# Optimization experiments

Hardware: AMD Instinct MI355X
Metric: run time of the kernel (lower is better)

## Reference

```python
import jax, jax.numpy as jnp
import numpy as np

B, T, DIM, NH = 2, 2048, 1024, 16
HD = DIM // NH  # 64


def setup_inputs() -> dict:
    key = jax.random.key(0)
    ks = jax.random.split(key, 5)
    x = jax.random.normal(ks[0], (B, T, DIM), dtype=jnp.float32)
    # realistic RoPE tables (any float tables work; use true rotary angles)
    inv_freq = 1.0 / (10000.0 ** (jnp.arange(0, HD, 2, dtype=jnp.float32) / HD))  # [HD/2]
    ang = jnp.arange(T, dtype=jnp.float32)[:, None] * inv_freq[None, :]           # [T, HD/2]
    ang = jnp.repeat(ang, 2, axis=-1)                                             # [T, HD] interleaved pairs
    sin = jnp.sin(ang)[None, None]  # [1,1,T,HD]
    cos = jnp.cos(ang)[None, None]
    W_qkv = jax.random.normal(ks[1], (DIM, 3 * DIM), dtype=jnp.float32) * (DIM ** -0.5)
    W_proj = jax.random.normal(ks[2], (DIM, DIM), dtype=jnp.float32) * (DIM ** -0.5)
    return {"x": x, "sin": sin, "cos": cos, "W_qkv": W_qkv, "W_proj": W_proj}


def _rope(x, sin, cos):
    # x: [B,H,T,D]; sin/cos: [1,1,T,D]
    x1, x2 = x[..., ::2], x[..., 1::2]
    xr = jnp.stack((-x2, x1), axis=-1).reshape(x.shape)  # interleave (-x2, x1)
    return x * cos + xr * sin


def reference(x, sin, cos, W_qkv, W_proj):
    Bx, Tx, C = x.shape
    nh, hd = NH, C // NH
    qkv = x @ W_qkv                                   # [B,T,3C]
    q, k, v = jnp.split(qkv, 3, axis=-1)
    to_bhtd = lambda t: t.reshape(Bx, Tx, nh, hd).transpose(0, 2, 1, 3)
    q, k, v = to_bhtd(q), to_bhtd(k), to_bhtd(v)      # [B,H,T,D]
    q = _rope(q, sin[:, :, :Tx], cos[:, :, :Tx])
    k = _rope(k, sin[:, :, :Tx], cos[:, :, :Tx])
    scale = 1.0 / jnp.sqrt(jnp.asarray(hd, dtype=x.dtype))
    scores = jnp.einsum('bhqd,bhkd->bhqk', q, k) * scale
    causal = jnp.tril(jnp.ones((Tx, Tx), dtype=bool))
    scores = jnp.where(causal, scores, jnp.finfo(scores.dtype).min)
    attn = jax.nn.softmax(scores, axis=-1)
    y = jnp.einsum('bhqk,bhkd->bhqd', attn, v)        # [B,H,T,D]
    y = y.transpose(0, 2, 1, 3).reshape(Bx, Tx, C)
    return y @ W_proj
```

## Files before the change

kernel.cpp:

```cpp
#include <hip/hip_runtime.h>


typedef float  f32x4  __attribute__((ext_vector_type(4)));
typedef __bf16 bf16x8 __attribute__((ext_vector_type(8)));
typedef short  short8 __attribute__((ext_vector_type(8)));

#define Bb   2
#define Tt   2048
#define DIMc 1024
#define NHh  16
#define HDd  64

__device__ __forceinline__ short f2bf(float f) {
    unsigned u = __builtin_bit_cast(unsigned, f);
    u += 0x7fffu + ((u >> 16) & 1u);
    return (short)(u >> 16);
}

__device__ __forceinline__ f32x4 mfma16(short8 a, short8 b, f32x4 c) {
    return __builtin_amdgcn_mfma_f32_16x16x32_bf16(
        __builtin_bit_cast(bf16x8, a), __builtin_bit_cast(bf16x8, b), c, 0, 0, 0);
}

__device__ __forceinline__ void gl_lds16(const void* g, void* l) {
    __builtin_amdgcn_global_load_lds(
        (const __attribute__((address_space(1))) unsigned int*)g,
        (__attribute__((address_space(3))) unsigned int*)l, 16, 0, 0);
}

__global__ __launch_bounds__(256) void convX(const float* __restrict__ X,
                                             short* __restrict__ Xb)
{
    size_t i = ((size_t)blockIdx.x * 256 + threadIdx.x) * 8;
    float4 a = *(const float4*)(X + i);
    float4 b = *(const float4*)(X + i + 4);
    short8 s;
    s[0] = f2bf(a.x); s[1] = f2bf(a.y); s[2] = f2bf(a.z); s[3] = f2bf(a.w);
    s[4] = f2bf(b.x); s[5] = f2bf(b.y); s[6] = f2bf(b.z); s[7] = f2bf(b.w);
    *(short8*)(Xb + i) = s;
}

__global__ __launch_bounds__(256) void convT(const float* __restrict__ W,
                                             short* __restrict__ Wt, int N)
{
    __shared__ float L[64][65];
    const int kb = blockIdx.x * 64, nb = blockIdx.y * 64;
    const int tid = threadIdx.x;
#pragma unroll
    for (int it = 0; it < 4; it++) {
        int kk = it * 16 + (tid >> 4), c = (tid & 15) * 4;
        float4 v = *(const float4*)(W + (size_t)(kb + kk) * N + nb + c);
        L[c + 0][kk] = v.x; L[c + 1][kk] = v.y;
        L[c + 2][kk] = v.z; L[c + 3][kk] = v.w;
    }
    __syncthreads();
#pragma unroll
    for (int it = 0; it < 2; it++) {
        int n = it * 32 + (tid >> 3), ks = (tid & 7) * 8;
        short8 s;
#pragma unroll
        for (int j = 0; j < 8; j++) s[j] = f2bf(L[n][ks + j]);
        *(short8*)(Wt + (size_t)(nb + n) * 1024 + kb + ks) = s;
    }
}

__global__ __launch_bounds__(256, 6) void qkv_rope(
    const short* __restrict__ A, const short* __restrict__ Bt,
    const float* __restrict__ Sn, const float* __restrict__ Cs,
    short* __restrict__ Qo, short* __restrict__ Ko, short* __restrict__ Vt)
{
    __shared__ __align__(16) short LP[64 * 64 + 128 * 64];
    short (*As)[64] = (short(*)[64])LP;
    short (*Bs)[64] = (short(*)[64])(LP + 64 * 64);

    const int bm = blockIdx.x, bn = blockIdx.y;
    const int tid = threadIdx.x;
    const int wv = tid >> 6, lane = tid & 63, g = lane >> 4, l16 = lane & 15;
    const int wr = wv >> 1, wc = wv & 1;
    const int sw = l16 & 7;

    f32x4 acc[2][4];
#pragma unroll
    for (int i = 0; i < 2; i++)
#pragma unroll
        for (int j = 0; j < 4; j++) acc[i][j] = (f32x4){0.f, 0.f, 0.f, 0.f};

    const int sr = tid >> 3, c8 = tid & 7;
    const int gc8 = (c8 ^ (sr & 7)) << 3;
    const short* pA = A  + (size_t)(bm * 64  + sr) * 1024 + gc8;
    const short* pB = Bt + (size_t)(bn * 128 + sr) * 1024 + gc8;

    for (int k0 = 0; k0 < 1024; k0 += 64) {
        gl_lds16(pA + k0,             &As[sr][c8 << 3]);
        gl_lds16(pA + k0 + 32 * 1024, &As[32 + sr][c8 << 3]);
        gl_lds16(pB + k0,             &Bs[sr][c8 << 3]);
        gl_lds16(pB + k0 + 32 * 1024, &Bs[32 + sr][c8 << 3]);
        gl_lds16(pB + k0 + 64 * 1024, &Bs[64 + sr][c8 << 3]);
        gl_lds16(pB + k0 + 96 * 1024, &Bs[96 + sr][c8 << 3]);
        __syncthreads();
#pragma unroll
        for (int ks = 0; ks < 2; ks++) {
            short8 af[2], bfr[4];
#pragma unroll
            for (int mt = 0; mt < 2; mt++)
                af[mt]  = *(const short8*)&As[wr * 32 + mt * 16 + l16][((ks * 4 + g) ^ sw) << 3];
#pragma unroll
            for (int nt = 0; nt < 4; nt++)
                bfr[nt] = *(const short8*)&Bs[wc * 64 + nt * 16 + l16][((ks * 4 + g) ^ sw) << 3];
#pragma unroll
            for (int mt = 0; mt < 2; mt++)
#pragma unroll
                for (int nt = 0; nt < 4; nt++) acc[mt][nt] = mfma16(af[mt], bfr[nt], acc[mt][nt]);
        }
        __syncthreads();
    }

    if (bn >= 16) {
        short (*T)[72] = (short(*)[72])LP;
        const int b  = bm >> 5;
        const int t0 = (bm * 64) & 2047;
        const int nbase = (bn - 16) * 128;
#pragma unroll
        for (int ch = 0; ch < 4; ++ch) {
            __syncthreads();
            if (wc == (ch >> 1)) {
#pragma unroll
                for (int ntl = 0; ntl < 2; ++ntl) {
                    int nt = (ch & 1) * 2 + ntl;
#pragma unroll
                    for (int mt = 0; mt < 2; ++mt)
#pragma unroll
                        for (int r = 0; r < 4; ++r)
                            T[ntl * 16 + l16][wr * 32 + mt * 16 + g * 4 + r] =
                                f2bf(acc[mt][nt][r]);
                }
            }
            __syncthreads();
            int row = tid >> 3, cc8 = (tid & 7) * 8;
            int nn = nbase + ch * 32 + row;
            int h = nn >> 6, d = nn & 63;
            short8 v0 = *(const short8*)&T[row][cc8];
            size_t base = (((size_t)(b * 16 + h) * 64 + d) << 11) + t0 + cc8;
            *(short8*)(Vt + base) = v0;
        }
    } else {
#pragma unroll
        for (int mt = 0; mt < 2; mt++)
#pragma unroll
            for (int nt = 0; nt < 4; nt++)
#pragma unroll
                for (int r = 0; r < 4; r++) {
                    int m = bm * 64 + wr * 32 + mt * 16 + g * 4 + r;
                    int n = bn * 128 + wc * 64 + nt * 16 + l16;
                    float val = acc[mt][nt][r];
                    float partner = __shfl_xor(val, 1, 64);
                    int b = m >> 11, t = m & 2047;
                    int sec = n >> 10, nn = n & 1023;
                    int h = nn >> 6, d = nn & 63;
                    float sv = Sn[t * 64 + d], cv = Cs[t * 64 + d];
                    float ro = (d & 1) ? fmaf(val, cv, partner * sv)
                                       : fmaf(val, cv, -partner * sv);
                    short* dst = (sec == 0) ? Qo : Ko;
                    dst[(((size_t)(b * 16 + h) << 11) + t) * 64 + d] = f2bf(ro);
                }
    }
}

__global__ __launch_bounds__(256, 4) void attn(
    const short* __restrict__ Q, const short* __restrict__ K,
    const short* __restrict__ V, short* __restrict__ Y)
{
    __shared__ __align__(16) short Ks[2][64][64];
    __shared__ __align__(16) short Vs[2][64][64];
    __shared__ __align__(16) short Pl[4][16][64];

    const int id = blockIdx.y * gridDim.x + blockIdx.x;
    const int bh = id >> 5;
    const int qi = ((id & 31) + ((id >> 8) << 3)) & 31;
    const int tid = threadIdx.x, wv = tid >> 6, lane = tid & 63;
    const int g = lane >> 4, l16 = lane & 15;
    const int q0w = qi * 64 + wv * 16;
    const short* Qb = Q + (size_t)bh * Tt * 64;
    const short* Kb = K + (size_t)bh * Tt * 64;
    const short* Vb = V + (size_t)bh * 64 * Tt;

    const int rj = lane >> 3, cc = lane & 7, gc = cc ^ rj;

    auto stage = [&](int s, int buf) {
        int k0s = s * 64;
#pragma unroll
        for (int j = 0; j < 2; j++) {
            int row = wv * 16 + j * 8 + rj;
            gl_lds16(Kb + (size_t)(k0s + row) * 64 + gc * 8, &Ks[buf][row][cc << 3]);
        }
#pragma unroll
        for (int j = 0; j < 2; j++) {
            int row = wv * 16 + j * 8 + rj;
            gl_lds16(Vb + (size_t)row * Tt + k0s + gc * 8, &Vs[buf][row][cc << 3]);
        }
    };

    short8 qf[2];
#pragma unroll
    for (int ss = 0; ss < 2; ss++)
        qf[ss] = *(const short8*)(Qb + (size_t)(q0w + l16) * 64 + ss * 32 + g * 8);

    f32x4 o[4];
#pragma unroll
    for (int nt = 0; nt < 4; nt++) o[nt] = (f32x4){0.f, 0.f, 0.f, 0.f};
    float lsum[4] = {0.f, 0.f, 0.f, 0.f};

    const int nsteps = qi + 1;
    const int sw = l16 & 7;

    stage(0, 0);
    __syncthreads();

    for (int s = 0; s < nsteps; ++s) {
        if (s + 1 < nsteps) stage(s + 1, (s + 1) & 1);
        const int kb = s & 1, k0 = s * 64;

        f32x4 S[4];
#pragma unroll
        for (int t = 0; t < 4; t++) {
            S[t] = (f32x4){0.f, 0.f, 0.f, 0.f};
#pragma unroll
            for (int ss = 0; ss < 2; ss++) {
                short8 kf = *(const short8*)&Ks[kb][t * 16 + l16][((ss * 4 + g) ^ sw) << 3];
                S[t] = mfma16(qf[ss], kf, S[t]);
            }
        }

        float p[4][4];
        if (s < nsteps - 1) {
#pragma unroll
            for (int t = 0; t < 4; t++)
#pragma unroll
                for (int r = 0; r < 4; r++)
                    p[t][r] = __expf(fmaf(S[t][r], 0.125f, -10.f));
        } else {
#pragma unroll
            for (int t = 0; t < 4; t++)
#pragma unroll
                for (int r = 0; r < 4; r++) {
                    int key = k0 + t * 16 + l16, qq = q0w + g * 4 + r;
                    p[t][r] = (key <= qq) ? __expf(fmaf(S[t][r], 0.125f, -10.f)) : 0.f;
                }
        }
#pragma unroll
        for (int r = 0; r < 4; r++)
            lsum[r] += (p[0][r] + p[1][r]) + (p[2][r] + p[3][r]);

#pragma unroll
        for (int t = 0; t < 4; t++)
#pragma unroll
            for (int r = 0; r < 4; r++) {
                int row = g * 4 + r, c = t * 16 + l16;
                Pl[wv][row][(((c >> 3) ^ (row & 7)) << 3) | (c & 7)] = f2bf(p[t][r]);
            }
        asm volatile("" ::: "memory");
        short8 pf[2];
#pragma unroll
        for (int ks = 0; ks < 2; ks++)
            pf[ks] = *(const short8*)&Pl[wv][l16][((ks * 4 + g) ^ sw) << 3];
#pragma unroll
        for (int nt = 0; nt < 4; nt++)
#pragma unroll
            for (int ks = 0; ks < 2; ks++) {
                short8 vf = *(const short8*)&Vs[kb][nt * 16 + l16][((ks * 4 + g) ^ sw) << 3];
                o[nt] = mfma16(pf[ks], vf, o[nt]);
            }
        __syncthreads();
    }

    float inv[4];
#pragma unroll
    for (int r = 0; r < 4; r++) {
        float t = lsum[r];
        t += __shfl_xor(t, 1, 64);
        t += __shfl_xor(t, 2, 64);
        t += __shfl_xor(t, 4, 64);
        t += __shfl_xor(t, 8, 64);
        inv[r] = 1.0f / t;
    }
    const int b = bh >> 4, h = bh & 15;
#pragma unroll
    for (int nt = 0; nt < 4; nt++)
#pragma unroll
        for (int r = 0; r < 4; r++) {
            int qq = q0w + g * 4 + r, d = nt * 16 + l16;
            Y[((size_t)(b * Tt + qq)) * DIMc + h * 64 + d] = f2bf(o[nt][r] * inv[r]);
        }
}

__global__ __launch_bounds__(256, 4) void proj(
    const short* __restrict__ A, const short* __restrict__ Bt, float* __restrict__ O)
{
    __shared__ __align__(16) short As[64][64];
    __shared__ __align__(16) short Bs[64][64];
    const int bm = blockIdx.x, bn = blockIdx.y;
    const int tid = threadIdx.x;
    const int wv = tid >> 6, lane = tid & 63, g = lane >> 4, l16 = lane & 15;
    const int wr = wv >> 1, wc = wv & 1;
    const int sw = l16 & 7;

    f32x4 acc[2][2];
#pragma unroll
    for (int i = 0; i < 2; i++)
#pragma unroll
        for (int j = 0; j < 2; j++) acc[i][j] = (f32x4){0.f, 0.f, 0.f, 0.f};

    const int sr = tid >> 3, c8 = tid & 7;
    const int gc8 = (c8 ^ (sr & 7)) << 3;
    const short* pA = A  + (size_t)(bm * 64 + sr) * 1024 + gc8;
    const short* pB = Bt + (size_t)(bn * 64 + sr) * 1024 + gc8;

    for (int k0 = 0; k0 < 1024; k0 += 64) {
        gl_lds16(pA + k0,             &As[sr][c8 << 3]);
        gl_lds16(pA + k0 + 32 * 1024, &As[32 + sr][c8 << 3]);
        gl_lds16(pB + k0,             &Bs[sr][c8 << 3]);
        gl_lds16(pB + k0 + 32 * 1024, &Bs[32 + sr][c8 << 3]);
        __syncthreads();
#pragma unroll
        for (int ks = 0; ks < 2; ks++) {
            short8 af[2], bfr[2];
#pragma unroll
            for (int mt = 0; mt < 2; mt++)
                af[mt]  = *(const short8*)&As[wr * 32 + mt * 16 + l16][((ks * 4 + g) ^ sw) << 3];
#pragma unroll
            for (int nt = 0; nt < 2; nt++)
                bfr[nt] = *(const short8*)&Bs[wc * 32 + nt * 16 + l16][((ks * 4 + g) ^ sw) << 3];
#pragma unroll
            for (int mt = 0; mt < 2; mt++)
#pragma unroll
                for (int nt = 0; nt < 2; nt++) acc[mt][nt] = mfma16(af[mt], bfr[nt], acc[mt][nt]);
        }
        __syncthreads();
    }

#pragma unroll
    for (int mt = 0; mt < 2; mt++)
#pragma unroll
        for (int nt = 0; nt < 2; nt++)
#pragma unroll
            for (int r = 0; r < 4; r++) {
                int m = bm * 64 + wr * 32 + mt * 16 + g * 4 + r;
                int n = bn * 64 + wc * 32 + nt * 16 + l16;
                O[(size_t)m * 1024 + n] = acc[mt][nt][r];
            }
}

extern "C" void kernel_launch(void* const* d_in, const int* in_sizes, int n_in,
                              void* d_out, int out_size, void* d_ws, size_t ws_size,
                              hipStream_t stream)
{
    const float* x     = (const float*)d_in[0];
    const float* sn    = (const float*)d_in[1];
    const float* cs    = (const float*)d_in[2];
    const float* wqkv  = (const float*)d_in[3];
    const float* wproj = (const float*)d_in[4];
    float* out = (float*)d_out;

    char* ws = (char*)d_ws;
    const size_t MB = 1024 * 1024;
    short* q   = (short*)(ws);
    short* k   = (short*)(ws + 8  * MB);
    short* vt  = (short*)(ws + 16 * MB);
    short* y   = (short*)(ws + 24 * MB);
    short* xb  = (short*)(ws + 32 * MB);
    short* wqt = (short*)(ws + 40 * MB);
    short* wpt = (short*)(ws + 46 * MB);

    convX<<<2048, 256, 0, stream>>>(x, xb);
    convT<<<dim3(16, 48), 256, 0, stream>>>(wqkv, wqt, 3072);
    convT<<<dim3(16, 16), 256, 0, stream>>>(wproj, wpt, 1024);
    qkv_rope<<<dim3(64, 24), 256, 0, stream>>>(xb, wqt, sn, cs, q, k, vt);
    attn<<<dim3(Tt / 64, Bb * NHh), 256, 0, stream>>>(q, k, vt, y);
    proj<<<dim3(64, 16), 256, 0, stream>>>(y, wpt, out);
}
```

Baseline: 188.0 us.

## Rewrite attention as single-wave 32x32 MFMA kernel with register-only P transpose

Each block of the attention kernel is now one 64-lane wave that handles 32 queries. It uses 32x32x16 bf16 MFMA and computes S transposed (K·Qᵀ) so that P can be packed with v_cvt_pk_bf16 and rearranged across lanes with permlane32_swap, with no LDS round trip. K and V fragments are loaded straight from global memory into registers, which removes the LDS staging, the double buffering and all __syncthreads. This cuts LDS traffic and barriers and raises block count and parallelism. In exchange it loses K/V reuse across waves and any software prefetch, so every wave re-reads K/V from global or L2 with load latency exposed.

After: 220.9 us. 1.18x slower.

```diff
diff --git a/kernel.cpp b/kernel.cpp
--- a/kernel.cpp
+++ b/kernel.cpp
@@ -1,9 +1,12 @@
 #include <hip/hip_runtime.h>
 
 
-typedef float  f32x4  __attribute__((ext_vector_type(4)));
-typedef __bf16 bf16x8 __attribute__((ext_vector_type(8)));
-typedef short  short8 __attribute__((ext_vector_type(8)));
+typedef float  f32x4   __attribute__((ext_vector_type(4)));
+typedef float  f32x16  __attribute__((ext_vector_type(16)));
+typedef __bf16 bf16x8  __attribute__((ext_vector_type(8)));
+typedef short  short8  __attribute__((ext_vector_type(8)));
+typedef unsigned uint2v __attribute__((ext_vector_type(2)));
+typedef unsigned uint4v __attribute__((ext_vector_type(4)));
 
 #define Bb   2
 #define Tt   2048
@@ -20,6 +23,17 @@
 __device__ __forceinline__ f32x4 mfma16(short8 a, short8 b, f32x4 c) {
     return __builtin_amdgcn_mfma_f32_16x16x32_bf16(
         __builtin_bit_cast(bf16x8, a), __builtin_bit_cast(bf16x8, b), c, 0, 0, 0);
+}
+
+__device__ __forceinline__ f32x16 mfma32(short8 a, short8 b, f32x16 c) {
+    return __builtin_amdgcn_mfma_f32_32x32x16_bf16(
+        __builtin_bit_cast(bf16x8, a), __builtin_bit_cast(bf16x8, b), c, 0, 0, 0);
+}
+
+__device__ __forceinline__ unsigned cvtpk(float lo, float hi) {
+    unsigned r;
+    asm("v_cvt_pk_bf16_f32 %0, %1, %2" : "=v"(r) : "v"(lo), "v"(hi));
+    return r;
 }
 
 __device__ __forceinline__ void gl_lds16(const void* g, void* l) {
@@ -166,131 +180,102 @@
     }
 }
 
-__global__ __launch_bounds__(256, 4) void attn(
+__global__ __launch_bounds__(64, 4) void attn(
     const short* __restrict__ Q, const short* __restrict__ K,
     const short* __restrict__ V, short* __restrict__ Y)
 {
-    __shared__ __align__(16) short Ks[2][64][64];
-    __shared__ __align__(16) short Vs[2][64][64];
-    __shared__ __align__(16) short Pl[4][16][64];
-
-    const int id = blockIdx.y * gridDim.x + blockIdx.x;
-    const int bh = id >> 5;
-    const int qi = ((id & 31) + ((id >> 8) << 3)) & 31;
-    const int tid = threadIdx.x, wv = tid >> 6, lane = tid & 63;
-    const int g = lane >> 4, l16 = lane & 15;
-    const int q0w = qi * 64 + wv * 16;
+    const int id = blockIdx.x;
+    const int bh = id >> 6;
+    const int qw = ((id & 63) + ((id >> 8) << 3)) & 63;
+    const int lane = threadIdx.x;
+    const int l5 = lane & 31, hi = lane >> 5;
+    const int q0 = qw * 32;
+    const int qabs = q0 + l5;
+
     const short* Qb = Q + (size_t)bh * Tt * 64;
     const short* Kb = K + (size_t)bh * Tt * 64;
     const short* Vb = V + (size_t)bh * 64 * Tt;
 
-    const int rj = lane >> 3, cc = lane & 7, gc = cc ^ rj;
-
-    auto stage = [&](int s, int buf) {
-        int k0s = s * 64;
-#pragma unroll
-        for (int j = 0; j < 2; j++) {
-            int row = wv * 16 + j * 8 + rj;
-            gl_lds16(Kb + (size_t)(k0s + row) * 64 + gc * 8, &Ks[buf][row][cc << 3]);
-        }
-#pragma unroll
-        for (int j = 0; j < 2; j++) {
-            int row = wv * 16 + j * 8 + rj;
-            gl_lds16(Vb + (size_t)row * Tt + k0s + gc * 8, &Vs[buf][row][cc << 3]);
-        }
-    };
-
-    short8 qf[2];
-#pragma unroll
-    for (int ss = 0; ss < 2; ss++)
-        qf[ss] = *(const short8*)(Qb + (size_t)(q0w + l16) * 64 + ss * 32 + g * 8);
-
-    f32x4 o[4];
-#pragma unroll
-    for (int nt = 0; nt < 4; nt++) o[nt] = (f32x4){0.f, 0.f, 0.f, 0.f};
-    float lsum[4] = {0.f, 0.f, 0.f, 0.f};
-
-    const int nsteps = qi + 1;
-    const int sw = l16 & 7;
-
-    stage(0, 0);
-    __syncthreads();
-
+    short8 qf[4];
+#pragma unroll
+    for (int c = 0; c < 4; c++)
+        qf[c] = *(const short8*)(Qb + (size_t)(q0 + l5) * 64 + c * 16 + hi * 8);
+
+    f32x16 o0, o1;
+    float lsum = 0.f;
+#pragma unroll
+    for (int r = 0; r < 16; r++) { o0[r] = 0.f; o1[r] = 0.f; }
+
+    const int nsteps = qw + 1;
     for (int s = 0; s < nsteps; ++s) {
-        if (s + 1 < nsteps) stage(s + 1, (s + 1) & 1);
-        const int kb = s & 1, k0 = s * 64;
-
-        f32x4 S[4];
+        const int k0 = s * 32;
+        const short* kp = Kb + (size_t)(k0 + l5) * 64 + hi * 8;
+        short8 kf0 = *(const short8*)(kp);
+        short8 kf1 = *(const short8*)(kp + 16);
+        short8 kf2 = *(const short8*)(kp + 32);
+        short8 kf3 = *(const short8*)(kp + 48);
+        const short* vp = Vb + (size_t)l5 * Tt + k0 + hi * 8;
+        short8 vf00 = *(const short8*)(vp);
+        short8 vf01 = *(const short8*)(vp + 16);
+        short8 vf10 = *(const short8*)(vp + 32 * Tt);
+        short8 vf11 = *(const short8*)(vp + 32 * Tt + 16);
+
+        f32x16 st;
+#pragma unroll
+        for (int r = 0; r < 16; r++) st[r] = 0.f;
+        st = mfma32(kf0, qf[0], st);
+        st = mfma32(kf1, qf[1], st);
+        st = mfma32(kf2, qf[2], st);
+        st = mfma32(kf3, qf[3], st);
+
+        float p[16];
+        if (s < nsteps - 1) {
+#pragma unroll
+            for (int r = 0; r < 16; r++)
+                p[r] = __expf(fmaf(st[r], 0.125f, -10.f));
+        } else {
+#pragma unroll
+            for (int r = 0; r < 16; r++) {
+                int key = k0 + (r & 3) + 8 * (r >> 2) + 4 * hi;
+                p[r] = (key <= qabs) ? __expf(fmaf(st[r], 0.125f, -10.f)) : 0.f;
+            }
+        }
+#pragma unroll
+        for (int r = 0; r < 16; r += 4)
+            lsum += (p[r] + p[r + 1]) + (p[r + 2] + p[r + 3]);
+
+        unsigned w[8];
 #pragma unroll
         for (int t = 0; t < 4; t++) {
-            S[t] = (f32x4){0.f, 0.f, 0.f, 0.f};
-#pragma unroll
-            for (int ss = 0; ss < 2; ss++) {
-                short8 kf = *(const short8*)&Ks[kb][t * 16 + l16][((ss * 4 + g) ^ sw) << 3];
-                S[t] = mfma16(qf[ss], kf, S[t]);
-            }
-        }
-
-        float p[4][4];
-        if (s < nsteps - 1) {
-#pragma unroll
-            for (int t = 0; t < 4; t++)
-#pragma unroll
-                for (int r = 0; r < 4; r++)
-                    p[t][r] = __expf(fmaf(S[t][r], 0.125f, -10.f));
-        } else {
-#pragma unroll
-            for (int t = 0; t < 4; t++)
-#pragma unroll
-                for (int r = 0; r < 4; r++) {
-                    int key = k0 + t * 16 + l16, qq = q0w + g * 4 + r;
-                    p[t][r] = (key <= qq) ? __expf(fmaf(S[t][r], 0.125f, -10.f)) : 0.f;
-                }
-        }
-#pragma unroll
-        for (int r = 0; r < 4; r++)
-            lsum[r] += (p[0][r] + p[1][r]) + (p[2][r] + p[3][r]);
-
-#pragma unroll
-        for (int t = 0; t < 4; t++)
-#pragma unroll
-            for (int r = 0; r < 4; r++) {
-                int row = g * 4 + r, c = t * 16 + l16;
-                Pl[wv][row][(((c >> 3) ^ (row & 7)) << 3) | (c & 7)] = f2bf(p[t][r]);
-            }
-        asm volatile("" ::: "memory");
-        short8 pf[2];
-#pragma unroll
-        for (int ks = 0; ks < 2; ks++)
-            pf[ks] = *(const short8*)&Pl[wv][l16][((ks * 4 + g) ^ sw) << 3];
-#pragma unroll
-        for (int nt = 0; nt < 4; nt++)
-#pragma unroll
-            for (int ks = 0; ks < 2; ks++) {
-                short8 vf = *(const short8*)&Vs[kb][nt * 16 + l16][((ks * 4 + g) ^ sw) << 3];
-                o[nt] = mfma16(pf[ks], vf, o[nt]);
-            }
-        __syncthreads();
-    }
-
-    float inv[4];
-#pragma unroll
-    for (int r = 0; r < 4; r++) {
-        float t = lsum[r];
-        t += __shfl_xor(t, 1, 64);
-        t += __shfl_xor(t, 2, 64);
-        t += __shfl_xor(t, 4, 64);
-        t += __shfl_xor(t, 8, 64);
-        inv[r] = 1.0f / t;
-    }
+            w[2 * t]     = cvtpk(p[4 * t],     p[4 * t + 1]);
+            w[2 * t + 1] = cvtpk(p[4 * t + 2], p[4 * t + 3]);
+        }
+        uint2v s0 = __builtin_amdgcn_permlane32_swap(w[0], w[2], false, false);
+        uint2v s1 = __builtin_amdgcn_permlane32_swap(w[1], w[3], false, false);
+        uint2v s2 = __builtin_amdgcn_permlane32_swap(w[4], w[6], false, false);
+        uint2v s3 = __builtin_amdgcn_permlane32_swap(w[5], w[7], false, false);
+        uint4v u0 = {s0[0], s1[0], s0[1], s1[1]};
+        uint4v u1 = {s2[0], s3[0], s2[1], s3[1]};
+        short8 pa0 = __builtin_bit_cast(short8, u0);
+        short8 pa1 = __builtin_bit_cast(short8, u1);
+
+        o0 = mfma32(pa0, vf00, o0);
+        o0 = mfma32(pa1, vf01, o0);
+        o1 = mfma32(pa0, vf10, o1);
+        o1 = mfma32(pa1, vf11, o1);
+    }
+
+    lsum += __shfl_xor(lsum, 32, 64);
+    float inv = 1.0f / lsum;
     const int b = bh >> 4, h = bh & 15;
 #pragma unroll
-    for (int nt = 0; nt < 4; nt++)
-#pragma unroll
-        for (int r = 0; r < 4; r++) {
-            int qq = q0w + g * 4 + r, d = nt * 16 + l16;
-            Y[((size_t)(b * Tt + qq)) * DIMc + h * 64 + d] = f2bf(o[nt][r] * inv[r]);
-        }
+    for (int r = 0; r < 16; r++) {
+        int ql = (r & 3) + 8 * (r >> 2) + 4 * hi;
+        float iv = __shfl(inv, ql, 64);
+        size_t row = ((size_t)(b * Tt + q0 + ql)) * DIMc + h * 64;
+        Y[row + l5]      = f2bf(o0[r] * iv);
+        Y[row + 32 + l5] = f2bf(o1[r] * iv);
+    }
 }
 
 __global__ __launch_bounds__(256, 4) void proj(
@@ -375,6 +360,6 @@
     convT<<<dim3(16, 48), 256, 0, stream>>>(wqkv, wqt, 3072);
     convT<<<dim3(16, 16), 256, 0, stream>>>(wproj, wpt, 1024);
     qkv_rope<<<dim3(64, 24), 256, 0, stream>>>(xb, wqt, sn, cs, q, k, vt);
-    attn<<<dim3(Tt / 64, Bb * NHh), 256, 0, stream>>>(q, k, vt, y);
+    attn<<<dim3(Tt / 32 * Bb * NHh), 64, 0, stream>>>(q, k, vt, y);
     proj<<<dim3(64, 16), 256, 0, stream>>>(y, wpt, out);
 }
```
